# Kernel tuning notes

Measured on AMD Instinct MI355X. Metric: run time of the kernel, lower is better.

The kernel has to match this reference:

```python
import jax, jax.numpy as jnp
import numpy as np


def conv1d(x, w, b, pad):
    # x: (B, Cin, T), w: (Cout, Cin, K), b: (Cout,)
    y = jax.lax.conv_general_dilated(x, w, window_strides=(1,), padding=[(pad, pad)],
                                     dimension_numbers=('NCH', 'OIH', 'NCH'))
    return y + b[None, :, None]


def setup_inputs() -> dict:
    key = jax.random.key(0)
    ks = jax.random.split(key, 16)
    B, Cmel, Ctxt, Catt, T1, T2 = 16, 80, 256, 80, 800, 200
    s = 0.05
    return {
        'queries': jax.random.normal(ks[0], (B, Cmel, T1), jnp.float32),
        'keys': jax.random.normal(ks[1], (B, Ctxt, T2), jnp.float32),
        'attn_prior': jax.random.uniform(ks[2], (B, T1, T2), jnp.float32),
        # key_proj: Conv1d(256->512,k=3,pad=1) -> ReLU -> Conv1d(512->80,k=1)
        'kw1': jax.random.normal(ks[3], (Ctxt * 2, Ctxt, 3), jnp.float32) * s,
        'kb1': jax.random.normal(ks[4], (Ctxt * 2,), jnp.float32) * s,
        'kw2': jax.random.normal(ks[5], (Catt, Ctxt * 2, 1), jnp.float32) * s,
        'kb2': jax.random.normal(ks[6], (Catt,), jnp.float32) * s,
        # query_proj (3xconv): 80->160 k3 -> ReLU -> 160->80 k1 -> ReLU -> 80->80 k1
        'qw1': jax.random.normal(ks[7], (Cmel * 2, Cmel, 3), jnp.float32) * s,
        'qb1': jax.random.normal(ks[8], (Cmel * 2,), jnp.float32) * s,
        'qw2': jax.random.normal(ks[9], (Cmel, Cmel * 2, 1), jnp.float32) * s,
        'qb2': jax.random.normal(ks[10], (Cmel,), jnp.float32) * s,
        'qw3': jax.random.normal(ks[11], (Catt, Cmel, 1), jnp.float32) * s,
        'qb3': jax.random.normal(ks[12], (Catt,), jnp.float32) * s,
    }


def reference(queries, keys, attn_prior, kw1, kb1, kw2, kb2, qw1, qb1, qw2, qb2, qw3, qb3):
    # key encoder
    k = jax.nn.relu(conv1d(keys, kw1, kb1, pad=1))
    k = conv1d(k, kw2, kb2, pad=0)                      # (B, Catt, T2)
    # query encoder ('3xconv')
    q = jax.nn.relu(conv1d(queries, qw1, qb1, pad=1))
    q = jax.nn.relu(conv1d(q, qw2, qb2, pad=0))
    q = conv1d(q, qw3, qb3, pad=0)                      # (B, Catt, T1)
    # L2 distance over channels: ||q||^2 + ||k||^2 - 2 q.k (same math as broadcast (q-k)^2 sum)
    q2 = jnp.sum(q * q, axis=1)                         # (B, T1)
    k2 = jnp.sum(k * k, axis=1)                         # (B, T2)
    qk = jnp.einsum('bct,bcs->bts', q, k)               # (B, T1, T2)
    attn = -0.0005 * (q2[:, :, None] + k2[:, None, :] - 2.0 * qk)[:, None]  # (B,1,T1,T2)
    attn = jax.nn.log_softmax(attn, axis=3) + jnp.log(attn_prior[:, None] + 1e-8)
    return attn
```

## Files before the change

kernel.cpp:

```cpp
#include <hip/hip_runtime.h>
#include <cstdint>
#include <cmath>

using short8  = __attribute__((ext_vector_type(8))) short;
using short4v = __attribute__((ext_vector_type(4))) short;
using floatx4 = __attribute__((ext_vector_type(4))) float;

__device__ __forceinline__ short f2bf(float f) {
  union { float f; unsigned u; } x; x.f = f;
  unsigned r = x.u + 0x7FFFu + ((x.u >> 16) & 1u);
  return (short)(r >> 16);
}

__device__ __forceinline__ float bf2f(short s) {
  union { unsigned u; float f; } x; x.u = ((unsigned)(unsigned short)s) << 16;
  return x.f;
}

__device__ __forceinline__ void gl_lds16(const short* g, short* l) {
  __builtin_amdgcn_global_load_lds(
      (const __attribute__((address_space(1))) void*)g,
      (__attribute__((address_space(3))) void*)l, 16, 0, 0);
}

__global__ __launch_bounds__(256) void prep_kernel(
    const float* __restrict__ keys, const float* __restrict__ queries,
    const float* __restrict__ kw1, const float* __restrict__ kw2,
    const float* __restrict__ qw1, const float* __restrict__ qw2,
    const float* __restrict__ qw3,
    short* __restrict__ kT0, short* __restrict__ qT0,
    short* __restrict__ w1, short* __restrict__ w2, short* __restrict__ w3,
    short* __restrict__ w4, short* __restrict__ w5)
{
  const int bid = blockIdx.x, tid = threadIdx.x;
  __shared__ float xs[32][65];

  if (bid < 1136) {
    const float* src; short* dst; int CIN, T, CP, bx, by, b;
    if (bid < 512) {
      src = keys; dst = kT0; CIN = 256; T = 200; CP = 256;
      bx = bid & 3; by = (bid >> 2) & 7; b = bid >> 5;
    } else {
      int b2 = bid - 512;
      src = queries; dst = qT0; CIN = 80; T = 800; CP = 96;
      bx = b2 % 13; by = (b2 / 13) % 3; b = b2 / 39;
    }
    const int t0 = bx * 64, ci0 = by * 32;
    for (int i = tid; i < 32 * 64; i += 256) {
      int row = i >> 6, col = i & 63;
      float v = 0.f;
      if (ci0 + row < CIN && t0 + col < T)
        v = src[((size_t)b * CIN + ci0 + row) * T + t0 + col];
      xs[row][col] = v;
    }
    __syncthreads();
    int t = tid >> 2, c8 = (tid & 3) * 8;
    if (t0 + t < T) {
      short8 o;
      #pragma unroll
      for (int j = 0; j < 8; ++j) o[j] = f2bf(xs[c8 + j][t]);
      *(short8*)&dst[((size_t)b * T + t0 + t) * CP + ci0 + c8] = o;
    }
  } else {
    int blk = bid - 1136;
    const float* src; short* dst; int base;
    int CoP, CiP, Cout, CIN, K; bool isW1 = false;
    if      (blk < 384) { src=kw1; dst=w1; base=0;   CoP=512; CiP=256; Cout=512; CIN=256; K=3; isW1=true; }
    else if (blk < 432) { src=kw2; dst=w2; base=384; CoP=96;  CiP=512; Cout=80;  CIN=512; K=1; }
    else if (blk < 486) { src=qw1; dst=w3; base=432; CoP=192; CiP=96;  Cout=160; CIN=80;  K=3; }
    else if (blk < 504) { src=qw2; dst=w4; base=486; CoP=96;  CiP=192; Cout=80;  CIN=160; K=1; }
    else                { src=qw3; dst=w5; base=504; CoP=96;  CiP=96;  Cout=80;  CIN=80;  K=1; }
    int tot = K * CoP * CiP;
    int b0 = (blk - base) * 1024;
    for (int e = 0; e < 4; ++e) {
      int gi = b0 + e * 256 + tid;
      if (gi < tot) {
        int dk  = gi / (CoP * CiP);
        int rem = gi - dk * (CoP * CiP);
        int co  = rem / CiP, ci = rem - (rem / CiP) * CiP;
        float v = (co < Cout && ci < CIN) ? src[((size_t)co * CIN + ci) * K + dk] : 0.f;
        int idx = gi;
        if (isW1) idx = (((ci >> 5) * 3 + dk) * 512 + co) * 32 + (ci & 31);
        dst[idx] = f2bf(v);
      }
    }
  }
}

__global__ __launch_bounds__(256) void conv_k3_kernel(
    const short* __restrict__ kT0, const short* __restrict__ qT0,
    const short* __restrict__ w1, const short* __restrict__ w3,
    const short* __restrict__ w4, const short* __restrict__ w5,
    const float* __restrict__ kb1, const float* __restrict__ qb1,
    const float* __restrict__ qb2, const float* __restrict__ qb3,
    short* __restrict__ kT1, short* __restrict__ qF)
{
  __shared__ __align__(16) short smem[23040];
  const int tid = threadIdx.x, wid = tid >> 6, lane = tid & 63;
  const int q = lane >> 4, m = lane & 15;

  if (blockIdx.x < 512) {
    const int blk = blockIdx.x;
    const int bb = blk >> 5, co0 = ((blk >> 2) & 7) * 64, t0 = (blk & 3) * 64;
    const int wy = wid >> 1, wx = wid & 1;
    const int wv = tid >> 6;

    floatx4 acc[2][2];
    #pragma unroll
    for (int i = 0; i < 2; ++i)
      #pragma unroll
      for (int j = 0; j < 2; ++j) acc[i][j] = (floatx4){0.f, 0.f, 0.f, 0.f};

    auto xload = [&](int c0s, int4& a, int4& bvv) {
      { int row = tid >> 2, g = tid & 3;
        int t = t0 + row - 1;
        a = (int4){0,0,0,0};
        if (t >= 0 && t < 200)
          a = *(const int4*)&kT0[((size_t)bb * 200 + t) * 256 + c0s * 32 + g * 8]; }
      bvv = (int4){0,0,0,0};
      if (tid < 8) {
        int i1 = tid + 256, row = i1 >> 2, g = i1 & 3;
        int t = t0 + row - 1;
        if (t >= 0 && t < 200)
          bvv = *(const int4*)&kT0[((size_t)bb * 200 + t) * 256 + c0s * 32 + g * 8];
      }
    };
    auto xstore = [&](const int4& a, const int4& bvv, int xoff) {
      { int row = tid >> 2, g = tid & 3; *(int4*)&smem[xoff + row * 40 + g * 8] = a; }
      if (tid < 8) { int i1 = tid + 256, row = i1 >> 2, g = i1 & 3;
        *(int4*)&smem[xoff + row * 40 + g * 8] = bvv; }
    };
    auto wissue = [&](int c0s, int aoff) {
      #pragma unroll
      for (int c = 0; c < 3; ++c) {
        const short* g = w1 + ((size_t)(c0s * 3 + c) * 512 + co0) * 32 + tid * 8;
        gl_lds16(g, &smem[aoff + c * 2048 + wv * 512]);
      }
    };

    { int4 a, bvv; xload(0, a, bvv); wissue(0, 5280); xstore(a, bvv, 0); }
    __syncthreads();

    int cur = 0;
    for (int c0 = 0; c0 < 8; ++c0) {
      const int xo = cur ? 2640 : 0;
      const int ao = cur ? 11424 : 5280;
      int4 xa, xb;
      if (c0 < 7) {
        wissue(c0 + 1, cur ? 5280 : 11424);
        xload(c0 + 1, xa, xb);
      }
      #pragma unroll
      for (int dk = 0; dk < 3; ++dk) {
        short8 fa0 = *(const short8*)&smem[ao + dk * 2048 + (wy * 32 + m) * 32 + q * 8];
        short8 fa1 = *(const short8*)&smem[ao + dk * 2048 + (wy * 32 + 16 + m) * 32 + q * 8];
        #pragma unroll
        for (int j = 0; j < 2; ++j) {
          short8 fb = *(const short8*)&smem[xo + (wx * 32 + j * 16 + m + dk) * 40 + q * 8];
          acc[0][j] = __builtin_amdgcn_mfma_f32_16x16x32_bf16(fa0, fb, acc[0][j], 0, 0, 0);
          acc[1][j] = __builtin_amdgcn_mfma_f32_16x16x32_bf16(fa1, fb, acc[1][j], 0, 0, 0);
        }
      }
      if (c0 < 7) {
        xstore(xa, xb, cur ? 0 : 2640);
        __syncthreads();
      }
      cur ^= 1;
    }
    #pragma unroll
    for (int i = 0; i < 2; ++i) {
      #pragma unroll
      for (int j = 0; j < 2; ++j) {
        #pragma unroll
        for (int r = 0; r < 4; ++r) {
          int co = co0 + wy * 32 + i * 16 + q * 4 + r;
          int t  = t0 + wx * 32 + j * 16 + m;
          if (t < 200) {
            float v = fmaxf(acc[i][j][r] + kb1[co], 0.f);
            kT1[((size_t)bb * 200 + t) * 512 + co] = f2bf(v);
          }
        }
      }
    }
  } else {
    const int qbid = blockIdx.x - 512;
    const int b = qbid / 13, t0 = (qbid % 13) * 64;
    short* xs2 = smem;
    short* y1c = smem + 7680;
    short* y2c = smem;

    floatx4 accq[3][4];
    #pragma unroll
    for (int f = 0; f < 3; ++f)
      #pragma unroll
      for (int tf = 0; tf < 4; ++tf) accq[f][tf] = (floatx4){0.f, 0.f, 0.f, 0.f};

    for (int i = tid; i < 66 * 12; i += 256) {
      int row = i / 12, g = i - (i / 12) * 12;
      int t = t0 + row - 1;
      int4 v = {0, 0, 0, 0};
      if (t >= 0 && t < 800)
        v = *(const int4*)&qT0[((size_t)b * 800 + t) * 96 + g * 8];
      *(int4*)&xs2[row * 104 + g * 8] = v;
    }
    __syncthreads();

    for (int c0 = 0; c0 < 3; ++c0) {
      #pragma unroll
      for (int dk = 0; dk < 3; ++dk) {
        short8 fa[3];
        #pragma unroll
        for (int f = 0; f < 3; ++f)
          fa[f] = *(const short8*)&w3[((size_t)(dk * 192 + wid * 48 + f * 16 + m)) * 96
                                      + c0 * 32 + q * 8];
        #pragma unroll
        for (int tf = 0; tf < 4; ++tf) {
          short8 fb = *(const short8*)&xs2[(tf * 16 + m + dk) * 104 + c0 * 32 + q * 8];
          #pragma unroll
          for (int f = 0; f < 3; ++f)
            accq[f][tf] = __builtin_amdgcn_mfma_f32_16x16x32_bf16(fa[f], fb, accq[f][tf], 0, 0, 0);
        }
      }
    }
    __syncthreads();
    #pragma unroll
    for (int f = 0; f < 3; ++f) {
      #pragma unroll
      for (int tf = 0; tf < 4; ++tf) {
        int co = wid * 48 + f * 16 + q * 4;
        int t  = tf * 16 + m;
        short4v o;
        #pragma unroll
        for (int r = 0; r < 4; ++r) {
          float bv = (co + r < 160) ? qb1[co + r] : 0.f;
          o[r] = f2bf(fmaxf(accq[f][tf][r] + bv, 0.f));
        }
        *(short4v*)&y1c[(co >> 5) * 2560 + t * 40 + (co & 31)] = o;
      }
    }
    __syncthreads();

    floatx4 acc2q[6];
    #pragma unroll
    for (int f = 0; f < 6; ++f) acc2q[f] = (floatx4){0.f, 0.f, 0.f, 0.f};
    #pragma unroll
    for (int c = 0; c < 6; ++c) {
      short8 fb = *(const short8*)&y1c[c * 2560 + (wid * 16 + m) * 40 + q * 8];
      #pragma unroll
      for (int f = 0; f < 6; ++f) {
        short8 fa = *(const short8*)&w4[((size_t)(f * 16 + m)) * 192 + c * 32 + q * 8];
        acc2q[f] = __builtin_amdgcn_mfma_f32_16x16x32_bf16(fa, fb, acc2q[f], 0, 0, 0);
      }
    }
    #pragma unroll
    for (int f = 0; f < 6; ++f) {
      int co = f * 16 + q * 4;
      int t  = wid * 16 + m;
      short4v o;
      #pragma unroll
      for (int r = 0; r < 4; ++r) {
        float bv = (co + r < 80) ? qb2[co + r] : 0.f;
        o[r] = f2bf(fmaxf(acc2q[f][r] + bv, 0.f));
      }
      *(short4v*)&y2c[(co >> 5) * 2560 + t * 40 + (co & 31)] = o;
    }
    __syncthreads();

    floatx4 acc3q[6];
    #pragma unroll
    for (int f = 0; f < 6; ++f) acc3q[f] = (floatx4){0.f, 0.f, 0.f, 0.f};
    #pragma unroll
    for (int c = 0; c < 3; ++c) {
      short8 fb = *(const short8*)&y2c[c * 2560 + (wid * 16 + m) * 40 + q * 8];
      #pragma unroll
      for (int f = 0; f < 6; ++f) {
        short8 fa = *(const short8*)&w5[((size_t)(f * 16 + m)) * 96 + c * 32 + q * 8];
        acc3q[f] = __builtin_amdgcn_mfma_f32_16x16x32_bf16(fa, fb, acc3q[f], 0, 0, 0);
      }
    }
    int t = t0 + wid * 16 + m;
    if (t < 800) {
      #pragma unroll
      for (int f = 0; f < 6; ++f) {
        int co = f * 16 + q * 4;
        short4v o;
        #pragma unroll
        for (int r = 0; r < 4; ++r) {
          float bv = (co + r < 80) ? qb3[co + r] : 0.f;
          o[r] = f2bf(acc3q[f][r] + bv);
        }
        *(short4v*)&qF[((size_t)b * 800 + t) * 96 + co] = o;
      }
    }
  }
}

__global__ __launch_bounds__(64) void kconv2_kernel(
    const short* __restrict__ kT1, const short* __restrict__ w2,
    const float* __restrict__ kb2, short* __restrict__ kF,
    float* __restrict__ k2g)
{
  const int blk = blockIdx.x;
  const int b = blk / 13, t0 = (blk - b * 13) * 16;
  const int lane = threadIdx.x & 63;
  const int q = lane >> 4, m = lane & 15;
  const int t = t0 + m;
  const bool tv = (t < 200);

  floatx4 acc[6];
  #pragma unroll
  for (int f = 0; f < 6; ++f) acc[f] = (floatx4){0.f, 0.f, 0.f, 0.f};

  #pragma unroll
  for (int c = 0; c < 16; ++c) {
    short8 fb;
    if (tv) fb = *(const short8*)&kT1[((size_t)b * 200 + t) * 512 + c * 32 + q * 8];
    else    fb = (short8){0,0,0,0,0,0,0,0};
    #pragma unroll
    for (int f = 0; f < 6; ++f) {
      short8 fa = *(const short8*)&w2[((size_t)(f * 16 + m)) * 512 + c * 32 + q * 8];
      acc[f] = __builtin_amdgcn_mfma_f32_16x16x32_bf16(fa, fb, acc[f], 0, 0, 0);
    }
  }
  if (tv) {
    float k2acc = 0.f;
    #pragma unroll
    for (int f = 0; f < 6; ++f) {
      int co = f * 16 + q * 4;
      short4v o;
      #pragma unroll
      for (int r = 0; r < 4; ++r) {
        float bv = (co + r < 80) ? kb2[co + r] : 0.f;
        short s = f2bf(acc[f][r] + bv);
        o[r] = s;
        float vb = bf2f(s);
        k2acc = fmaf(vb, vb, k2acc);
      }
      *(short4v*)&kF[((size_t)b * 200 + t) * 96 + co] = o;
    }
    k2acc += __shfl_xor(k2acc, 16);
    k2acc += __shfl_xor(k2acc, 32);
    if (q == 0) k2g[b * 200 + t] = k2acc;
  }
}

__global__ __launch_bounds__(128) void attn_mfma(
    const short* __restrict__ qT, const short* __restrict__ kT,
    const float* __restrict__ k2g, const float* __restrict__ prior,
    float* __restrict__ out)
{
  const int b = blockIdx.y, t1_0 = blockIdx.x * 32;
  const int tid = threadIdx.x, wid = tid >> 6, lane = tid & 63;
  const int q = lane >> 4, m = lane & 15;

  __shared__ __align__(16) char smem[25600];
  short* aq = (short*)smem;
  short* bk = (short*)(smem + 6656);
  float* sstage = (float*)smem;

  floatx4 acc[13];
  #pragma unroll
  for (int f = 0; f < 13; ++f) acc[f] = (floatx4){0.f, 0.f, 0.f, 0.f};

  for (int i = tid; i < 32 * 12; i += 128) {
    int row = i / 12, g = i - (i / 12) * 12;
    *(int4*)&aq[row * 104 + g * 8] =
        *(const int4*)&qT[((size_t)b * 800 + t1_0 + row) * 96 + g * 8];
  }

  for (int c = 0; c < 3; ++c) {
    __syncthreads();
    for (int i = tid; i < 208 * 4; i += 128) {
      int row = i >> 2, g = i & 3;
      int4 v = {0, 0, 0, 0};
      if (row < 200)
        v = *(const int4*)&kT[((size_t)b * 200 + row) * 96 + c * 32 + g * 8];
      *(int4*)&bk[row * 40 + g * 8] = v;
    }
    __syncthreads();
    short8 fa = *(const short8*)&aq[(wid * 16 + m) * 104 + c * 32 + q * 8];
    #pragma unroll
    for (int f = 0; f < 13; ++f) {
      short8 fb = *(const short8*)&bk[(f * 16 + m) * 40 + q * 8];
      acc[f] = __builtin_amdgcn_mfma_f32_16x16x32_bf16(fa, fb, acc[f], 0, 0, 0);
    }
  }

  float k2v[13];
  #pragma unroll
  for (int f = 0; f < 13; ++f) {
    int col = f * 16 + m;
    k2v[f] = (col < 200) ? k2g[b * 200 + col] : 0.f;
  }

  float mx[4] = {-INFINITY, -INFINITY, -INFINITY, -INFINITY};
  #pragma unroll
  for (int f = 0; f < 13; ++f) {
    bool valid = (f * 16 + m) < 200;
    #pragma unroll
    for (int r = 0; r < 4; ++r) {
      float v = valid ? (0.001f * acc[f][r] - 0.0005f * k2v[f]) : -INFINITY;
      acc[f][r] = v;
      mx[r] = fmaxf(mx[r], v);
    }
  }
  #pragma unroll
  for (int msk = 1; msk < 16; msk <<= 1)
    #pragma unroll
    for (int r = 0; r < 4; ++r) mx[r] = fmaxf(mx[r], __shfl_xor(mx[r], msk));
  float sm[4] = {0.f, 0.f, 0.f, 0.f};
  #pragma unroll
  for (int f = 0; f < 13; ++f)
    #pragma unroll
    for (int r = 0; r < 4; ++r) sm[r] += __expf(acc[f][r] - mx[r]);
  #pragma unroll
  for (int msk = 1; msk < 16; msk <<= 1)
    #pragma unroll
    for (int r = 0; r < 4; ++r) sm[r] += __shfl_xor(sm[r], msk);
  float lse[4];
  #pragma unroll
  for (int r = 0; r < 4; ++r) lse[r] = mx[r] + __logf(sm[r]);

  __syncthreads();
  #pragma unroll
  for (int f = 0; f < 13; ++f) {
    int col = f * 16 + m;
    if (col < 200) {
      #pragma unroll
      for (int r = 0; r < 4; ++r)
        sstage[(wid * 16 + q * 4 + r) * 200 + col] = acc[f][r] - lse[r];
    }
  }
  __syncthreads();

  for (int i = tid; i < 32 * 50; i += 128) {
    int row = i / 50, seg = i - (i / 50) * 50;
    size_t o = ((size_t)b * 800 + t1_0 + row) * 200 + seg * 4;
    floatx4 pv = *(const floatx4*)&prior[o];
    floatx4 sv = *(const floatx4*)&sstage[row * 200 + seg * 4];
    floatx4 ov;
    #pragma unroll
    for (int j = 0; j < 4; ++j) ov[j] = sv[j] + __logf(pv[j] + 1e-8f);
    *(floatx4*)&out[o] = ov;
  }
}

extern "C" void kernel_launch(void* const* d_in, const int* in_sizes, int n_in,
                              void* d_out, int out_size, void* d_ws, size_t ws_size,
                              hipStream_t stream) {
  const float* queries = (const float*)d_in[0];
  const float* keys    = (const float*)d_in[1];
  const float* prior   = (const float*)d_in[2];
  const float* kw1 = (const float*)d_in[3];
  const float* kb1 = (const float*)d_in[4];
  const float* kw2 = (const float*)d_in[5];
  const float* kb2 = (const float*)d_in[6];
  const float* qw1 = (const float*)d_in[7];
  const float* qb1 = (const float*)d_in[8];
  const float* qw2 = (const float*)d_in[9];
  const float* qb2 = (const float*)d_in[10];
  const float* qw3 = (const float*)d_in[11];
  const float* qb3 = (const float*)d_in[12];
  float* out = (float*)d_out;

  short* p = (short*)d_ws;
  short* kT0 = p;  p += (size_t)3200 * 256;
  short* qT0 = p;  p += (size_t)12800 * 96;
  short* w1  = p;  p += (size_t)3 * 512 * 256;
  short* w2  = p;  p += (size_t)96 * 512;
  short* w3  = p;  p += (size_t)3 * 192 * 96;
  short* w4  = p;  p += (size_t)96 * 192;
  short* w5  = p;  p += (size_t)96 * 96;
  short* kT1 = p;  p += (size_t)3200 * 512;
  short* kF  = p;  p += (size_t)3200 * 96;
  short* qF  = p;  p += (size_t)12800 * 96;
  float* k2g = (float*)p;

  prep_kernel<<<dim3(1649), 256, 0, stream>>>(keys, queries, kw1, kw2, qw1, qw2, qw3,
                                              kT0, qT0, w1, w2, w3, w4, w5);
  conv_k3_kernel<<<dim3(720), 256, 0, stream>>>(kT0, qT0, w1, w3, w4, w5,
                                                kb1, qb1, qb2, qb3, kT1, qF);
  kconv2_kernel<<<dim3(208), 64, 0, stream>>>(kT1, w2, kb2, kF, k2g);
  attn_mfma<<<dim3(25, 16), 128, 0, stream>>>(qF, kF, k2g, prior, out);
}
```

Before: 141.3 us.

## Fuse four pipeline kernels into one persistent kernel with grid barriers

Merges the prep, conv, key-conv2 and attention kernels into a single 720-block kernel. The stages are separated by atomic-counter grid barriers, and a memset resets the counters before each launch. The aim is to remove three kernel launch gaps and tail effects. In exchange, the attention and kconv2 stages run on only a fraction of the blocks. The barrier also depends on all 720 blocks being co-resident, which is not guaranteed and could deadlock.

```diff
diff --git a/kernel.cpp b/kernel.cpp
--- a/kernel.cpp
+++ b/kernel.cpp
@@ -23,85 +23,99 @@
       (__attribute__((address_space(3))) void*)l, 16, 0, 0);
 }
 
-__global__ __launch_bounds__(256) void prep_kernel(
-    const float* __restrict__ keys, const float* __restrict__ queries,
-    const float* __restrict__ kw1, const float* __restrict__ kw2,
-    const float* __restrict__ qw1, const float* __restrict__ qw2,
-    const float* __restrict__ qw3,
+#define NBLK 720
+
+__device__ __forceinline__ void grid_barrier(unsigned* cnt) {
+  __syncthreads();
+  if (threadIdx.x == 0) {
+    __threadfence();
+    atomicAdd(cnt, 1u);
+    while (atomicAdd(cnt, 0u) < (unsigned)NBLK) __builtin_amdgcn_s_sleep(8);
+    __threadfence();
+  }
+  __syncthreads();
+}
+
+__global__ __launch_bounds__(256, 3) void mega_kernel(
+    const float* __restrict__ queries, const float* __restrict__ keys,
+    const float* __restrict__ prior,
+    const float* __restrict__ kw1, const float* __restrict__ kb1,
+    const float* __restrict__ kw2, const float* __restrict__ kb2,
+    const float* __restrict__ qw1, const float* __restrict__ qb1,
+    const float* __restrict__ qw2, const float* __restrict__ qb2,
+    const float* __restrict__ qw3, const float* __restrict__ qb3,
     short* __restrict__ kT0, short* __restrict__ qT0,
     short* __restrict__ w1, short* __restrict__ w2, short* __restrict__ w3,
-    short* __restrict__ w4, short* __restrict__ w5)
+    short* __restrict__ w4, short* __restrict__ w5,
+    short* __restrict__ kT1, short* __restrict__ kF, short* __restrict__ qF,
+    float* __restrict__ k2g, unsigned* __restrict__ cnt,
+    float* __restrict__ out)
 {
-  const int bid = blockIdx.x, tid = threadIdx.x;
-  __shared__ float xs[32][65];
-
-  if (bid < 1136) {
-    const float* src; short* dst; int CIN, T, CP, bx, by, b;
-    if (bid < 512) {
-      src = keys; dst = kT0; CIN = 256; T = 200; CP = 256;
-      bx = bid & 3; by = (bid >> 2) & 7; b = bid >> 5;
-    } else {
-      int b2 = bid - 512;
-      src = queries; dst = qT0; CIN = 80; T = 800; CP = 96;
-      bx = b2 % 13; by = (b2 / 13) % 3; b = b2 / 39;
-    }
-    const int t0 = bx * 64, ci0 = by * 32;
-    for (int i = tid; i < 32 * 64; i += 256) {
-      int row = i >> 6, col = i & 63;
-      float v = 0.f;
-      if (ci0 + row < CIN && t0 + col < T)
-        v = src[((size_t)b * CIN + ci0 + row) * T + t0 + col];
-      xs[row][col] = v;
-    }
-    __syncthreads();
-    int t = tid >> 2, c8 = (tid & 3) * 8;
-    if (t0 + t < T) {
-      short8 o;
-      #pragma unroll
-      for (int j = 0; j < 8; ++j) o[j] = f2bf(xs[c8 + j][t]);
-      *(short8*)&dst[((size_t)b * T + t0 + t) * CP + ci0 + c8] = o;
-    }
-  } else {
-    int blk = bid - 1136;
-    const float* src; short* dst; int base;
-    int CoP, CiP, Cout, CIN, K; bool isW1 = false;
-    if      (blk < 384) { src=kw1; dst=w1; base=0;   CoP=512; CiP=256; Cout=512; CIN=256; K=3; isW1=true; }
-    else if (blk < 432) { src=kw2; dst=w2; base=384; CoP=96;  CiP=512; Cout=80;  CIN=512; K=1; }
-    else if (blk < 486) { src=qw1; dst=w3; base=432; CoP=192; CiP=96;  Cout=160; CIN=80;  K=3; }
-    else if (blk < 504) { src=qw2; dst=w4; base=486; CoP=96;  CiP=192; Cout=80;  CIN=160; K=1; }
-    else                { src=qw3; dst=w5; base=504; CoP=96;  CiP=96;  Cout=80;  CIN=80;  K=1; }
-    int tot = K * CoP * CiP;
-    int b0 = (blk - base) * 1024;
-    for (int e = 0; e < 4; ++e) {
-      int gi = b0 + e * 256 + tid;
-      if (gi < tot) {
-        int dk  = gi / (CoP * CiP);
-        int rem = gi - dk * (CoP * CiP);
-        int co  = rem / CiP, ci = rem - (rem / CiP) * CiP;
-        float v = (co < Cout && ci < CIN) ? src[((size_t)co * CIN + ci) * K + dk] : 0.f;
-        int idx = gi;
-        if (isW1) idx = (((ci >> 5) * 3 + dk) * 512 + co) * 32 + (ci & 31);
-        dst[idx] = f2bf(v);
+  __shared__ __align__(16) short smem[25600];
+  const int tid = threadIdx.x, bid = blockIdx.x;
+  const int wid = tid >> 6, lane = tid & 63;
+  const int q = lane >> 4, m = lane & 15;
+
+  {
+    float* xs = (float*)smem;
+    for (int u = bid; u < 1649; u += NBLK) {
+      if (u < 1136) {
+        const float* src; short* dst; int CIN, T, CP, bx, by, b;
+        if (u < 512) {
+          src = keys; dst = kT0; CIN = 256; T = 200; CP = 256;
+          bx = u & 3; by = (u >> 2) & 7; b = u >> 5;
+        } else {
+          int b2 = u - 512;
+          src = queries; dst = qT0; CIN = 80; T = 800; CP = 96;
+          bx = b2 % 13; by = (b2 / 13) % 3; b = b2 / 39;
+        }
+        const int t0 = bx * 64, ci0 = by * 32;
+        for (int i = tid; i < 32 * 64; i += 256) {
+          int row = i >> 6, col = i & 63;
+          float v = 0.f;
+          if (ci0 + row < CIN && t0 + col < T)
+            v = src[((size_t)b * CIN + ci0 + row) * T + t0 + col];
+          xs[row * 65 + col] = v;
+        }
+        __syncthreads();
+        int t = tid >> 2, c8 = (tid & 3) * 8;
+        if (t0 + t < T) {
+          short8 o;
+          #pragma unroll
+          for (int j = 0; j < 8; ++j) o[j] = f2bf(xs[(c8 + j) * 65 + t]);
+          *(short8*)&dst[((size_t)b * T + t0 + t) * CP + ci0 + c8] = o;
+        }
+        __syncthreads();
+      } else {
+        int blk = u - 1136;
+        const float* src; short* dst; int base;
+        int CoP, CiP, Cout, CIN, K; bool isW1 = false;
+        if      (blk < 384) { src=kw1; dst=w1; base=0;   CoP=512; CiP=256; Cout=512; CIN=256; K=3; isW1=true; }
+        else if (blk < 432) { src=kw2; dst=w2; base=384; CoP=96;  CiP=512; Cout=80;  CIN=512; K=1; }
+        else if (blk < 486) { src=qw1; dst=w3; base=432; CoP=192; CiP=96;  Cout=160; CIN=80;  K=3; }
+        else if (blk < 504) { src=qw2; dst=w4; base=486; CoP=96;  CiP=192; Cout=80;  CIN=160; K=1; }
+        else                { src=qw3; dst=w5; base=504; CoP=96;  CiP=96;  Cout=80;  CIN=80;  K=1; }
+        int tot = K * CoP * CiP;
+        int b0 = (blk - base) * 1024;
+        for (int e = 0; e < 4; ++e) {
+          int gi = b0 + e * 256 + tid;
+          if (gi < tot) {
+            int dk  = gi / (CoP * CiP);
+            int rem = gi - dk * (CoP * CiP);
+            int co  = rem / CiP, ci = rem - (rem / CiP) * CiP;
+            float v = (co < Cout && ci < CIN) ? src[((size_t)co * CIN + ci) * K + dk] : 0.f;
+            int idx = gi;
+            if (isW1) idx = (((ci >> 5) * 3 + dk) * 512 + co) * 32 + (ci & 31);
+            dst[idx] = f2bf(v);
+          }
+        }
       }
     }
   }
-}
-
-__global__ __launch_bounds__(256) void conv_k3_kernel(
-    const short* __restrict__ kT0, const short* __restrict__ qT0,
-    const short* __restrict__ w1, const short* __restrict__ w3,
-    const short* __restrict__ w4, const short* __restrict__ w5,
-    const float* __restrict__ kb1, const float* __restrict__ qb1,
-    const float* __restrict__ qb2, const float* __restrict__ qb3,
-    short* __restrict__ kT1, short* __restrict__ qF)
-{
-  __shared__ __align__(16) short smem[23040];
-  const int tid = threadIdx.x, wid = tid >> 6, lane = tid & 63;
-  const int q = lane >> 4, m = lane & 15;
-
-  if (blockIdx.x < 512) {
-    const int blk = blockIdx.x;
-    const int bb = blk >> 5, co0 = ((blk >> 2) & 7) * 64, t0 = (blk & 3) * 64;
+  grid_barrier(cnt + 0);
+
+  if (bid < 512) {
+    const int bb = bid >> 5, co0 = ((bid >> 2) & 7) * 64, t0 = (bid & 3) * 64;
     const int wy = wid >> 1, wx = wid & 1;
     const int wv = tid >> 6;
 
@@ -183,7 +197,7 @@
       }
     }
   } else {
-    const int qbid = blockIdx.x - 512;
+    const int qbid = bid - 512;
     const int b = qbid / 13, t0 = (qbid % 13) * 64;
     short* xs2 = smem;
     short* y1c = smem + 7680;
@@ -293,155 +307,151 @@
       }
     }
   }
-}
-
-__global__ __launch_bounds__(64) void kconv2_kernel(
-    const short* __restrict__ kT1, const short* __restrict__ w2,
-    const float* __restrict__ kb2, short* __restrict__ kF,
-    float* __restrict__ k2g)
-{
-  const int blk = blockIdx.x;
-  const int b = blk / 13, t0 = (blk - b * 13) * 16;
-  const int lane = threadIdx.x & 63;
-  const int q = lane >> 4, m = lane & 15;
-  const int t = t0 + m;
-  const bool tv = (t < 200);
-
-  floatx4 acc[6];
-  #pragma unroll
-  for (int f = 0; f < 6; ++f) acc[f] = (floatx4){0.f, 0.f, 0.f, 0.f};
-
-  #pragma unroll
-  for (int c = 0; c < 16; ++c) {
-    short8 fb;
-    if (tv) fb = *(const short8*)&kT1[((size_t)b * 200 + t) * 512 + c * 32 + q * 8];
-    else    fb = (short8){0,0,0,0,0,0,0,0};
-    #pragma unroll
-    for (int f = 0; f < 6; ++f) {
-      short8 fa = *(const short8*)&w2[((size_t)(f * 16 + m)) * 512 + c * 32 + q * 8];
-      acc[f] = __builtin_amdgcn_mfma_f32_16x16x32_bf16(fa, fb, acc[f], 0, 0, 0);
+  grid_barrier(cnt + 1);
+
+  {
+    int w = bid * 4 + wid;
+    if (w < 208) {
+      const int b = w / 13, t0 = (w - b * 13) * 16;
+      const int t = t0 + m;
+      const bool tv = (t < 200);
+
+      floatx4 acc[6];
+      #pragma unroll
+      for (int f = 0; f < 6; ++f) acc[f] = (floatx4){0.f, 0.f, 0.f, 0.f};
+
+      #pragma unroll
+      for (int c = 0; c < 16; ++c) {
+        short8 fb;
+        if (tv) fb = *(const short8*)&kT1[((size_t)b * 200 + t) * 512 + c * 32 + q * 8];
+        else    fb = (short8){0,0,0,0,0,0,0,0};
+        #pragma unroll
+        for (int f = 0; f < 6; ++f) {
+          short8 fa = *(const short8*)&w2[((size_t)(f * 16 + m)) * 512 + c * 32 + q * 8];
+          acc[f] = __builtin_amdgcn_mfma_f32_16x16x32_bf16(fa, fb, acc[f], 0, 0, 0);
+        }
+      }
+      if (tv) {
+        float k2acc = 0.f;
+        #pragma unroll
+        for (int f = 0; f < 6; ++f) {
+          int co = f * 16 + q * 4;
+          short4v o;
+          #pragma unroll
+          for (int r = 0; r < 4; ++r) {
+            float bv = (co + r < 80) ? kb2[co + r] : 0.f;
+            short s = f2bf(acc[f][r] + bv);
+            o[r] = s;
+            float vb = bf2f(s);
+            k2acc = fmaf(vb, vb, k2acc);
+          }
+          *(short4v*)&kF[((size_t)b * 200 + t) * 96 + co] = o;
+        }
+        k2acc += __shfl_xor(k2acc, 16);
+        k2acc += __shfl_xor(k2acc, 32);
+        if (q == 0) k2g[b * 200 + t] = k2acc;
+      }
     }
   }
-  if (tv) {
-    float k2acc = 0.f;
-    #pragma unroll
-    for (int f = 0; f < 6; ++f) {
-      int co = f * 16 + q * 4;
-      short4v o;
+  grid_barrier(cnt + 2);
+
+  if (bid < 200) {
+    const int half = tid >> 7, htid = tid & 127;
+    const int hwid = htid >> 6;
+    const int hl = htid & 63;
+    const int hq = hl >> 4, hm = hl & 15;
+    const int tile = bid * 2 + half;
+    const int b = tile / 25, t1_0 = (tile % 25) * 32;
+
+    short* aq = smem + half * 12800;
+    short* bk = smem + half * 12800 + 3328;
+    float* sstage = (float*)(smem + half * 12800);
+
+    floatx4 acc[13];
+    #pragma unroll
+    for (int f = 0; f < 13; ++f) acc[f] = (floatx4){0.f, 0.f, 0.f, 0.f};
+
+    for (int i = htid; i < 32 * 12; i += 128) {
+      int row = i / 12, g = i - (i / 12) * 12;
+      *(int4*)&aq[row * 104 + g * 8] =
+          *(const int4*)&qF[((size_t)b * 800 + t1_0 + row) * 96 + g * 8];
+    }
+
+    for (int c = 0; c < 3; ++c) {
+      __syncthreads();
+      for (int i = htid; i < 208 * 4; i += 128) {
+        int row = i >> 2, g = i & 3;
+        int4 v = {0, 0, 0, 0};
+        if (row < 200)
+          v = *(const int4*)&kF[((size_t)b * 200 + row) * 96 + c * 32 + g * 8];
+        *(int4*)&bk[row * 40 + g * 8] = v;
+      }
+      __syncthreads();
+      short8 fa = *(const short8*)&aq[(hwid * 16 + hm) * 104 + c * 32 + hq * 8];
+      #pragma unroll
+      for (int f = 0; f < 13; ++f) {
+        short8 fb = *(const short8*)&bk[(f * 16 + hm) * 40 + hq * 8];
+        acc[f] = __builtin_amdgcn_mfma_f32_16x16x32_bf16(fa, fb, acc[f], 0, 0, 0);
+      }
+    }
+
+    float k2v[13];
+    #pragma unroll
+    for (int f = 0; f < 13; ++f) {
+      int col = f * 16 + hm;
+      k2v[f] = (col < 200) ? k2g[b * 200 + col] : 0.f;
+    }
+
+    float mx[4] = {-INFINITY, -INFINITY, -INFINITY, -INFINITY};
+    #pragma unroll
+    for (int f = 0; f < 13; ++f) {
+      bool valid = (f * 16 + hm) < 200;
       #pragma unroll
       for (int r = 0; r < 4; ++r) {
-        float bv = (co + r < 80) ? kb2[co + r] : 0.f;
-        short s = f2bf(acc[f][r] + bv);
-        o[r] = s;
-        float vb = bf2f(s);
-        k2acc = fmaf(vb, vb, k2acc);
-      }
-      *(short4v*)&kF[((size_t)b * 200 + t) * 96 + co] = o;
-    }
-    k2acc += __shfl_xor(k2acc, 16);
-    k2acc += __shfl_xor(k2acc, 32);
-    if (q == 0) k2g[b * 200 + t] = k2acc;
-  }
-}
-
-__global__ __launch_bounds__(128) void attn_mfma(
-    const short* __restrict__ qT, const short* __restrict__ kT,
-    const float* __restrict__ k2g, const float* __restrict__ prior,
-    float* __restrict__ out)
-{
-  const int b = blockIdx.y, t1_0 = blockIdx.x * 32;
-  const int tid = threadIdx.x, wid = tid >> 6, lane = tid & 63;
-  const int q = lane >> 4, m = lane & 15;
-
-  __shared__ __align__(16) char smem[25600];
-  short* aq = (short*)smem;
-  short* bk = (short*)(smem + 6656);
-  float* sstage = (float*)smem;
-
-  floatx4 acc[13];
-  #pragma unroll
-  for (int f = 0; f < 13; ++f) acc[f] = (floatx4){0.f, 0.f, 0.f, 0.f};
-
-  for (int i = tid; i < 32 * 12; i += 128) {
-    int row = i / 12, g = i - (i / 12) * 12;
-    *(int4*)&aq[row * 104 + g * 8] =
-        *(const int4*)&qT[((size_t)b * 800 + t1_0 + row) * 96 + g * 8];
-  }
-
-  for (int c = 0; c < 3; ++c) {
-    __syncthreads();
-    for (int i = tid; i < 208 * 4; i += 128) {
-      int row = i >> 2, g = i & 3;
-      int4 v = {0, 0, 0, 0};
-      if (row < 200)
-        v = *(const int4*)&kT[((size_t)b * 200 + row) * 96 + c * 32 + g * 8];
-      *(int4*)&bk[row * 40 + g * 8] = v;
-    }
-    __syncthreads();
-    short8 fa = *(const short8*)&aq[(wid * 16 + m) * 104 + c * 32 + q * 8];
+        float v = valid ? (0.001f * acc[f][r] - 0.0005f * k2v[f]) : -INFINITY;
+        acc[f][r] = v;
+        mx[r] = fmaxf(mx[r], v);
+      }
+    }
+    #pragma unroll
+    for (int msk = 1; msk < 16; msk <<= 1)
+      #pragma unroll
+      for (int r = 0; r < 4; ++r) mx[r] = fmaxf(mx[r], __shfl_xor(mx[r], msk));
+    float sm[4] = {0.f, 0.f, 0.f, 0.f};
+    #pragma unroll
+    for (int f = 0; f < 13; ++f)
+      #pragma unroll
+      for (int r = 0; r < 4; ++r) sm[r] += __expf(acc[f][r] - mx[r]);
+    #pragma unroll
+    for (int msk = 1; msk < 16; msk <<= 1)
+      #pragma unroll
+      for (int r = 0; r < 4; ++r) sm[r] += __shfl_xor(sm[r], msk);
+    float lse[4];
+    #pragma unroll
+    for (int r = 0; r < 4; ++r) lse[r] = mx[r] + __logf(sm[r]);
+
+    __syncthreads();
     #pragma unroll
     for (int f = 0; f < 13; ++f) {
-      short8 fb = *(const short8*)&bk[(f * 16 + m) * 40 + q * 8];
-      acc[f] = __builtin_amdgcn_mfma_f32_16x16x32_bf16(fa, fb, acc[f], 0, 0, 0);
-    }
-  }
-
-  float k2v[13];
-  #pragma unroll
-  for (int f = 0; f < 13; ++f) {
-    int col = f * 16 + m;
-    k2v[f] = (col < 200) ? k2g[b * 200 + col] : 0.f;
-  }
-
-  float mx[4] = {-INFINITY, -INFINITY, -INFINITY, -INFINITY};
-  #pragma unroll
-  for (int f = 0; f < 13; ++f) {
-    bool valid = (f * 16 + m) < 200;
-    #pragma unroll
-    for (int r = 0; r < 4; ++r) {
-      float v = valid ? (0.001f * acc[f][r] - 0.0005f * k2v[f]) : -INFINITY;
-      acc[f][r] = v;
-      mx[r] = fmaxf(mx[r], v);
-    }
-  }
-  #pragma unroll
-  for (int msk = 1; msk < 16; msk <<= 1)
-    #pragma unroll
-    for (int r = 0; r < 4; ++r) mx[r] = fmaxf(mx[r], __shfl_xor(mx[r], msk));
-  float sm[4] = {0.f, 0.f, 0.f, 0.f};
-  #pragma unroll
-  for (int f = 0; f < 13; ++f)
-    #pragma unroll
-    for (int r = 0; r < 4; ++r) sm[r] += __expf(acc[f][r] - mx[r]);
-  #pragma unroll
-  for (int msk = 1; msk < 16; msk <<= 1)
-    #pragma unroll
-    for (int r = 0; r < 4; ++r) sm[r] += __shfl_xor(sm[r], msk);
-  float lse[4];
-  #pragma unroll
-  for (int r = 0; r < 4; ++r) lse[r] = mx[r] + __logf(sm[r]);
-
-  __syncthreads();
-  #pragma unroll
-  for (int f = 0; f < 13; ++f) {
-    int col = f * 16 + m;
-    if (col < 200) {
-      #pragma unroll
-      for (int r = 0; r < 4; ++r)
-        sstage[(wid * 16 + q * 4 + r) * 200 + col] = acc[f][r] - lse[r];
-    }
-  }
-  __syncthreads();
-
-  for (int i = tid; i < 32 * 50; i += 128) {
-    int row = i / 50, seg = i - (i / 50) * 50;
-    size_t o = ((size_t)b * 800 + t1_0 + row) * 200 + seg * 4;
-    floatx4 pv = *(const floatx4*)&prior[o];
-    floatx4 sv = *(const floatx4*)&sstage[row * 200 + seg * 4];
-    floatx4 ov;
-    #pragma unroll
-    for (int j = 0; j < 4; ++j) ov[j] = sv[j] + __logf(pv[j] + 1e-8f);
-    *(floatx4*)&out[o] = ov;
+      int col = f * 16 + hm;
+      if (col < 200) {
+        #pragma unroll
+        for (int r = 0; r < 4; ++r)
+          sstage[(hwid * 16 + hq * 4 + r) * 200 + col] = acc[f][r] - lse[r];
+      }
+    }
+    __syncthreads();
+
+    for (int i = htid; i < 32 * 50; i += 128) {
+      int row = i / 50, seg = i - (i / 50) * 50;
+      size_t o = ((size_t)b * 800 + t1_0 + row) * 200 + seg * 4;
+      floatx4 pv = *(const floatx4*)&prior[o];
+      floatx4 sv = *(const floatx4*)&sstage[row * 200 + seg * 4];
+      floatx4 ov;
+      #pragma unroll
+      for (int j = 0; j < 4; ++j) ov[j] = sv[j] + __logf(pv[j] + 1e-8f);
+      *(floatx4*)&out[o] = ov;
+    }
   }
 }
 
@@ -475,11 +485,12 @@
   short* kF  = p;  p += (size_t)3200 * 96;
   short* qF  = p;  p += (size_t)12800 * 96;
   float* k2g = (float*)p;
-
-  prep_kernel<<<dim3(1649), 256, 0, stream>>>(keys, queries, kw1, kw2, qw1, qw2, qw3,
-                                              kT0, qT0, w1, w2, w3, w4, w5);
-  conv_k3_kernel<<<dim3(720), 256, 0, stream>>>(kT0, qT0, w1, w3, w4, w5,
-                                                kb1, qb1, qb2, qb3, kT1, qF);
-  kconv2_kernel<<<dim3(208), 64, 0, stream>>>(kT1, w2, kb2, kF, k2g);
-  attn_mfma<<<dim3(25, 16), 128, 0, stream>>>(qF, kF, k2g, prior, out);
-}
+  unsigned* cnt = (unsigned*)(k2g + 3200);
+
+  hipMemsetAsync(cnt, 0, 3 * sizeof(unsigned), stream);
+  mega_kernel<<<dim3(NBLK), dim3(256), 0, stream>>>(
+      queries, keys, prior, kw1, kb1, kw2, kb2,
+      qw1, qb1, qw2, qb2, qw3, qb3,
+      kT0, qT0, w1, w2, w3, w4, w5,
+      kT1, kF, qF, k2g, cnt, out);
+}
```

Result: slower. 365.2 us (+158.5%).
